# Optimization experiments

Measured on AMD Instinct MI355X. Metric: run time of the kernel, lower is better.

Reference implementation:

```python
import jax, jax.numpy as jnp
import numpy as np

N, D, K = 10000, 784, 16          # nodes, input feat dim, num_neighbors
E = N * (K - 1)                   # edges
H = 128                           # hidden width in all MLPs
SIZES = [784, 128, 2]             # node_sizes


def setup_inputs() -> dict:
    key = jax.random.key(0)
    ks = jax.random.split(key, 24)
    w = lambda k, shape: jax.random.normal(k, shape, jnp.float32) * 0.02
    inp = {
        "x": jax.random.normal(ks[0], (N, D), jnp.float32),
        "edge_attr": jax.random.uniform(ks[1], (E, 1), jnp.float32),
        "idxs": jax.random.randint(ks[2], (N, K - 1), 0, N, dtype=jnp.int32),
    }
    # Layer 1: in=784, msg_size=784, out=128
    inp["l1_msg_w1"] = w(ks[3], (D + 1, H));      inp["l1_msg_b1"] = jnp.zeros((H,), jnp.float32)
    inp["l1_msg_w2"] = w(ks[4], (H, D));          inp["l1_msg_b2"] = jnp.zeros((D,), jnp.float32)
    inp["l1_node_w1"] = w(ks[5], (D + D, H));     inp["l1_node_b1"] = jnp.zeros((H,), jnp.float32)
    inp["l1_node_w2"] = w(ks[6], (H, 128));       inp["l1_node_b2"] = jnp.zeros((128,), jnp.float32)
    # Layer 2: in=128, msg_size=128, out=2
    inp["l2_msg_w1"] = w(ks[7], (128 + 1, H));    inp["l2_msg_b1"] = jnp.zeros((H,), jnp.float32)
    inp["l2_msg_w2"] = w(ks[8], (H, 128));        inp["l2_msg_b2"] = jnp.zeros((128,), jnp.float32)
    inp["l2_node_w1"] = w(ks[9], (128 + 128, H)); inp["l2_node_b1"] = jnp.zeros((H,), jnp.float32)
    inp["l2_node_w2"] = w(ks[10], (H, 2));        inp["l2_node_b2"] = jnp.zeros((2,), jnp.float32)
    return inp


def _mlp(x, w1, b1, w2, b2):
    return jax.nn.relu(x @ w1 + b1) @ w2 + b2


def _node_layer(x, src, edge_attr,
                mw1, mb1, mw2, mb2, nw1, nb1, nw2, nb2):
    # message over edges: cat(x[src], edge_attr) -> MLP   [E, msg_size]
    msg = _mlp(jnp.concatenate([x[src], edge_attr], axis=1), mw1, mb1, mw2, mb2)
    # scatter_mean by src index (faithful to the original, which uses index=src)
    sums = jax.ops.segment_sum(msg, src, num_segments=N)
    cnt = jax.ops.segment_sum(jnp.ones((src.shape[0], 1), msg.dtype), src, num_segments=N)
    agg = jnp.where(cnt > 0, sums / jnp.maximum(cnt, 1.0), 0.0)
    # node update: cat(x, agg_msg) -> MLP
    return _mlp(jnp.concatenate([x, agg], axis=1), nw1, nb1, nw2, nb2)


def reference(x, edge_attr, idxs,
              l1_msg_w1, l1_msg_b1, l1_msg_w2, l1_msg_b2,
              l1_node_w1, l1_node_b1, l1_node_w2, l1_node_b2,
              l2_msg_w1, l2_msg_b1, l2_msg_w2, l2_msg_b2,
              l2_node_w1, l2_node_b1, l2_node_w2, l2_node_b2):
    src = idxs.reshape(-1)  # [E]; dst is unused by the original message computation
    h = _node_layer(x, src, edge_attr,
                    l1_msg_w1, l1_msg_b1, l1_msg_w2, l1_msg_b2,
                    l1_node_w1, l1_node_b1, l1_node_w2, l1_node_b2)
    proj = _node_layer(h, src, edge_attr,
                       l2_msg_w1, l2_msg_b1, l2_msg_w2, l2_msg_b2,
                       l2_node_w1, l2_node_b1, l2_node_w2, l2_node_b2)  # [N, 2]
    # vectorized per-neighbor squared distances (replaces the nested python loop)
    neigh = proj[idxs]                                   # [N, K-1, 2]
    d = jnp.sum((proj[:, None, :] - neigh) ** 2, axis=-1)  # [N, K-1]
    return d.reshape(-1, 1)                              # [N*(K-1), 1]
```

## Files before the change

### kernel.cpp

```cpp
#include <hip/hip_runtime.h>

#define N_NODES 10000
#define E_EDGES 150000
#define KNB     15
#define EBLOCKS 587
#define GEMMB   626

typedef unsigned short u16;
typedef __bf16 bf16x8 __attribute__((ext_vector_type(8)));
typedef float  f32x4  __attribute__((ext_vector_type(4)));

__device__ __forceinline__ void split3(float a, u16& h, u16& m, u16& l) {
    unsigned u = __float_as_uint(a);
    unsigned t = u + 0x7FFFu + ((u >> 16) & 1u);
    h = (u16)(t >> 16);
    float r1 = a - __uint_as_float(t & 0xFFFF0000u);
    unsigned u1 = __float_as_uint(r1);
    m = (u16)(u1 >> 16);
    float r2 = r1 - __uint_as_float(u1 & 0xFFFF0000u);
    l = (u16)(__float_as_uint(r2) >> 16);
}

__global__ void count_kernel(const int* __restrict__ idxs, int* __restrict__ cnt, int e) {
    int i = blockIdx.x * blockDim.x + threadIdx.x;
    if (i < e) atomicAdd(&cnt[idxs[i]], 1);
}

__device__ __forceinline__
void gemm_tile2(const float* __restrict__ A, int K,
                const float* __restrict__ Blo, const float* __restrict__ Bhi, int ldB,
                float* __restrict__ C, int ldC, int M,
                int rowBlk, int colBlk) {
    __shared__ float As2[16][34];
    __shared__ float Bs2[16][64];
    int tid = threadIdx.x;
    int tn  = tid & 15, tm = tid >> 4;
    int arow = tid >> 3, acB = (tid & 7) << 1;
    int brow = tid >> 4, bcol = (tid & 15) << 2;
    int rowBase = rowBlk * 32, colBase = colBlk * 64;

    bool half = (Bhi != nullptr) && (colBase >= 128);
    const float* B = half ? Bhi : Blo;
    int bj = colBase - (half ? 128 : 0) + bcol;

    float2 av; float4 bv;
    auto loadA = [&](int k0, float2& dst) {
        int gr = rowBase + arow;
        if (gr < M) dst = *(const float2*)(A + (size_t)gr * K + k0 + acB);
        else { dst.x = dst.y = 0.f; }
    };
    auto loadB = [&](int k0, float4& dst) {
        dst = *(const float4*)(B + (size_t)(k0 + brow) * ldB + bj);
    };
    loadA(0, av); loadB(0, bv);

    float acc[2][4] = {};
    for (int k0 = 0; k0 < K; k0 += 16) {
        __syncthreads();
        As2[acB + 0][arow] = av.x; As2[acB + 1][arow] = av.y;
        *(float4*)&Bs2[brow][bcol] = bv;
        __syncthreads();
        if (k0 + 16 < K) { loadA(k0 + 16, av); loadB(k0 + 16, bv); }
#pragma unroll
        for (int k = 0; k < 16; ++k) {
            float4 b = *(const float4*)&Bs2[k][tn << 2];
            float2 a = *(const float2*)&As2[k][tm << 1];
            acc[0][0] = fmaf(a.x, b.x, acc[0][0]); acc[0][1] = fmaf(a.x, b.y, acc[0][1]);
            acc[0][2] = fmaf(a.x, b.z, acc[0][2]); acc[0][3] = fmaf(a.x, b.w, acc[0][3]);
            acc[1][0] = fmaf(a.y, b.x, acc[1][0]); acc[1][1] = fmaf(a.y, b.y, acc[1][1]);
            acc[1][2] = fmaf(a.y, b.z, acc[1][2]); acc[1][3] = fmaf(a.y, b.w, acc[1][3]);
        }
    }
#pragma unroll
    for (int i = 0; i < 2; ++i) {
        int row = rowBase + tm * 2 + i;
        if (row >= M) continue;
#pragma unroll
        for (int j = 0; j < 4; ++j)
            C[(size_t)row * ldC + colBase + (tn << 2) + j] = acc[i][j];
    }
}

__global__ __launch_bounds__(256)
void scanfold_kernel(const float* __restrict__ mw2, const float* __restrict__ mb2,
                     const float* __restrict__ nw1, const float* __restrict__ nb2,
                     const float* __restrict__ nw2,
                     const float* __restrict__ m2w1, const float* __restrict__ m2b1,
                     const float* __restrict__ m2w2, const float* __restrict__ m2b2,
                     const float* __restrict__ n2w1, const float* __restrict__ n2b1,
                     float* __restrict__ M1, float* __restrict__ M2,
                     float* __restrict__ WH,
                     float* __restrict__ v1, float* __restrict__ v2,
                     float* __restrict__ bu2, float* __restrict__ bx2,
                     const int* __restrict__ cnt, int* __restrict__ eoff,
                     float* __restrict__ maskv, int* __restrict__ fillc,
                     const float* __restrict__ mw1, u16* __restrict__ Bt) {
    int b = blockIdx.x;
    if (b >= 41) {
        __shared__ float Lt[800][17];
        int b2 = b - 41;
        int colBase = b2 * 16;
        const float* S = (colBase < 128) ? mw1 : nw1;
        int sc = colBase & 127;
        int tid = threadIdx.x;
        for (int i = 0; i < 50; ++i) {
            int row = (tid >> 4) + i * 16;
            Lt[row][tid & 15] = (row < 784) ? S[(size_t)row * 128 + sc + (tid & 15)] : 0.f;
        }
        __syncthreads();
        int col = tid >> 4, o = tid & 15;
        size_t dbase = (size_t)(colBase + col) * 800;
        for (int o2 = o; o2 < 100; o2 += 16) {
            u16 hs[8], ms[8], ls[8];
#pragma unroll
            for (int e = 0; e < 8; ++e) split3(Lt[o2 * 8 + e][col], hs[e], ms[e], ls[e]);
            auto pk = [](const u16* s) {
                uint4 v;
                v.x = s[0] | ((unsigned)s[1] << 16); v.y = s[2] | ((unsigned)s[3] << 16);
                v.z = s[4] | ((unsigned)s[5] << 16); v.w = s[6] | ((unsigned)s[7] << 16);
                return v;
            };
            *(uint4*)(Bt +          dbase + o2 * 8) = pk(hs);
            *(uint4*)(Bt + 204800 + dbase + o2 * 8) = pk(ms);
            *(uint4*)(Bt + 409600 + dbase + o2 * 8) = pk(ls);
        }
        return;
    }
    if (b == 0) {
        __shared__ int ssum[256];
        int tid = threadIdx.x;
        const int CH = 40;
        int base = tid * CH;
        int v[CH]; int s = 0;
#pragma unroll
        for (int q = 0; q < CH; ++q) {
            int i = base + q;
            v[q] = (i < N_NODES) ? cnt[i] : 0;
            s += v[q];
        }
        ssum[tid] = s;
        __syncthreads();
        for (int off = 1; off < 256; off <<= 1) {
            int t = (tid >= off) ? ssum[tid - off] : 0;
            __syncthreads();
            ssum[tid] += t;
            __syncthreads();
        }
        int ex = ssum[tid] - s;
#pragma unroll
        for (int q = 0; q < CH; ++q) {
            int i = base + q;
            if (i < N_NODES) {
                eoff[i]  = ex;
                maskv[i] = (v[q] > 0) ? 1.f : 0.f;
                fillc[i] = 0;
                ex += v[q];
            }
        }
        return;
    }
    b -= 1;
    if (b < 8) {
        gemm_tile2(mw2, 784, nw1 + 784 * 128, nullptr, 128, M1, 128, 128, b >> 1, b & 1);
    } else if (b < 16) {
        int t = b - 8;
        gemm_tile2(m2w2, 128, n2w1 + 128 * 128, nullptr, 128, M2, 128, 128, t >> 1, t & 1);
    } else if (b < 32) {
        int t = b - 16;
        gemm_tile2(nw2, 128, m2w1, n2w1, 128, WH, 256, 128, t >> 2, t & 3);
    } else {
        __shared__ float red[256];
        int t  = (b - 32) >> 1;
        int j  = ((b - 32) & 1) * 64 + (threadIdx.x & 63);
        int kq = threadIdx.x >> 6;
        const float* bvec; const float* Bv; const float* add; float* out; int Kv;
        if (t == 0)      { bvec = mb2;  Bv = nw1 + 784 * 128;  add = nullptr; out = v1;  Kv = 784; }
        else if (t == 1) { bvec = m2b2; Bv = n2w1 + 128 * 128; add = nullptr; out = v2;  Kv = 128; }
        else if (t == 2) { bvec = nb2;  Bv = m2w1;             add = m2b1;    out = bu2; Kv = 128; }
        else             { bvec = nb2;  Bv = n2w1;             add = n2b1;    out = bx2; Kv = 128; }
        float acc = 0.f;
        for (int k = kq; k < Kv; k += 4) acc = fmaf(bvec[k], Bv[k * 128 + j], acc);
        red[threadIdx.x] = acc;
        __syncthreads();
        if (threadIdx.x < 64) {
            float tot = red[threadIdx.x] + red[threadIdx.x + 64] +
                        red[threadIdx.x + 128] + red[threadIdx.x + 192];
            out[j] = tot + (add ? add[j] : 0.f);
        }
    }
}

#define MF(a, b, c) __builtin_amdgcn_mfma_f32_16x16x32_bf16((a), (b), (c), 0, 0, 0)

__device__ __forceinline__
void gemm_mfma(const float* __restrict__ A, const u16* __restrict__ Bt,
               const float* __restrict__ biasLo, const float* __restrict__ biasHi,
               const float* __restrict__ vhi, const float* __restrict__ rowmask,
               float* __restrict__ C, int gb) {
    __shared__ u16 Bs[3][8][64][8];
    __shared__ u16 As[3][2][64][8];
    const int tid  = threadIdx.x;
    const int lane = tid & 63, w = tid >> 6;
    const int rb = gb >> 1, cb = gb & 1;
    const int rowBase = rb * 32, colBase = cb * 128;

    const int ar  = tid >> 3;
    const int akc = (tid & 7) << 2;
    int arow = rowBase + ar; if (arow > N_NODES - 1) arow = N_NODES - 1;
    const float* Ap = A + (size_t)arow * 784;
    const int aL  = (ar & 15) + ((akc >> 3) << 4);
    const int aE  = akc & 4;
    u16* aDst = &As[0][ar >> 4][aL][aE];

    u16* bBase = &Bs[0][0][lane][0];
#define BDEF(j) \
    const int pl##j = (w * 6 + j) >> 3, cf##j = (w * 6 + j) & 7; \
    const int bofs##j = pl##j * 204800 + (colBase + cf##j * 16 + (lane & 15)) * 800 + ((lane >> 4) << 3); \
    const int bd##j = (pl##j * 8 + cf##j) * 512; \
    uint4 bv##j;
    BDEF(0) BDEF(1) BDEF(2) BDEF(3) BDEF(4) BDEF(5)
#undef BDEF

    float4 av;
    ushort4 a3h, a3m, a3l;

#define ALOAD(k0) { int kk = akc + (k0); if (kk >= 784) kk = 0; \
                    av = *(const float4*)(Ap + kk); }
#define BLOADALL(k0) \
    bv0 = *(const uint4*)(Bt + bofs0 + (k0)); \
    bv1 = *(const uint4*)(Bt + bofs1 + (k0)); \
    bv2 = *(const uint4*)(Bt + bofs2 + (k0)); \
    bv3 = *(const uint4*)(Bt + bofs3 + (k0)); \
    bv4 = *(const uint4*)(Bt + bofs4 + (k0)); \
    bv5 = *(const uint4*)(Bt + bofs5 + (k0));
#define ASPLIT() { u16 h, m, l; \
    split3(av.x, h, m, l); a3h.x = h; a3m.x = m; a3l.x = l; \
    split3(av.y, h, m, l); a3h.y = h; a3m.y = m; a3l.y = l; \
    split3(av.z, h, m, l); a3h.z = h; a3m.z = m; a3l.z = l; \
    split3(av.w, h, m, l); a3h.w = h; a3m.w = m; a3l.w = l; }

    f32x4 acc00 = {0.f, 0.f, 0.f, 0.f};
    f32x4 acc01 = acc00, acc10 = acc00, acc11 = acc00;

    ALOAD(0) BLOADALL(0) ASPLIT()

    const u16* aFr = &As[0][0][lane][0];
    const u16* bFr = &Bs[0][w * 2][lane][0];

    for (int t = 0; t < 25; ++t) {
        __syncthreads();
        *(ushort4*)(aDst)        = a3h;
        *(ushort4*)(aDst + 1024) = a3m;
        *(ushort4*)(aDst + 2048) = a3l;
        *(uint4*)(bBase + bd0) = bv0;
        *(uint4*)(bBase + bd1) = bv1;
        *(uint4*)(bBase + bd2) = bv2;
        *(uint4*)(bBase + bd3) = bv3;
        *(uint4*)(bBase + bd4) = bv4;
        *(uint4*)(bBase + bd5) = bv5;
        __syncthreads();
        const int kn = (t + 1) << 5;
        if (t < 24) { ALOAD(kn) BLOADALL(kn) }

        bf16x8 a0h = *(const bf16x8*)(aFr);
        bf16x8 a1h = *(const bf16x8*)(aFr + 512);
        bf16x8 a0m = *(const bf16x8*)(aFr + 1024);
        bf16x8 a1m = *(const bf16x8*)(aFr + 1536);
        bf16x8 a0l = *(const bf16x8*)(aFr + 2048);
        bf16x8 a1l = *(const bf16x8*)(aFr + 2560);

        bf16x8 bb0 = *(const bf16x8*)(bFr);
        bf16x8 bb1 = *(const bf16x8*)(bFr + 512);
        acc00 = MF(a0h, bb0, acc00); acc01 = MF(a0h, bb1, acc01);
        acc10 = MF(a1h, bb0, acc10); acc11 = MF(a1h, bb1, acc11);
        acc00 = MF(a0m, bb0, acc00); acc01 = MF(a0m, bb1, acc01);
        acc10 = MF(a1m, bb0, acc10); acc11 = MF(a1m, bb1, acc11);
        acc00 = MF(a0l, bb0, acc00); acc01 = MF(a0l, bb1, acc01);
        acc10 = MF(a1l, bb0, acc10); acc11 = MF(a1l, bb1, acc11);
        bf16x8 bc0 = *(const bf16x8*)(bFr + 4096);
        bf16x8 bc1 = *(const bf16x8*)(bFr + 4608);
        acc00 = MF(a0h, bc0, acc00); acc01 = MF(a0h, bc1, acc01);
        acc10 = MF(a1h, bc0, acc10); acc11 = MF(a1h, bc1, acc11);
        acc00 = MF(a0m, bc0, acc00); acc01 = MF(a0m, bc1, acc01);
        acc10 = MF(a1m, bc0, acc10); acc11 = MF(a1m, bc1, acc11);
        bf16x8 bdq0 = *(const bf16x8*)(bFr + 8192);
        bf16x8 bdq1 = *(const bf16x8*)(bFr + 8704);
        acc00 = MF(a0h, bdq0, acc00); acc01 = MF(a0h, bdq1, acc01);
        acc10 = MF(a1h, bdq0, acc10); acc11 = MF(a1h, bdq1, acc11);

        if (t < 24) ASPLIT()
    }
#undef ALOAD
#undef BLOADALL
#undef ASPLIT

    const float* bias = cb ? biasHi : biasLo;
#define EPI(rf, cf, ACC) { \
        const int col = colBase + w * 32 + (cf) * 16 + (lane & 15); \
        const int cj  = col & 127; \
        const float bb = bias[cj]; \
        const float vh = cb ? vhi[cj] : 0.f; \
        const int rbase = rowBase + (rf) * 16 + ((lane >> 4) << 2); \
        _Pragma("unroll") \
        for (int r = 0; r < 4; ++r) { \
            int row = rbase + r; \
            if (row < N_NODES) { \
                float v = ACC[r] + bb; \
                if (cb) v = fmaf(rowmask[row], vh, v); \
                C[(size_t)row * 256 + col] = v; \
            } } }
    EPI(0, 0, acc00) EPI(0, 1, acc01) EPI(1, 0, acc10) EPI(1, 1, acc11)
#undef EPI
}

__global__ __launch_bounds__(256)
void fillgemm_kernel(const int* __restrict__ idxs, const float* __restrict__ ea,
                     const int* __restrict__ eoff, int* __restrict__ fillc,
                     float* __restrict__ eas,
                     const float* __restrict__ A, const u16* __restrict__ Bt,
                     const float* __restrict__ biasLo, const float* __restrict__ biasHi,
                     const float* __restrict__ vhi, const float* __restrict__ rowmask,
                     float* __restrict__ C) {
    int gb = blockIdx.x;
    if (gb < GEMMB) {
        gemm_mfma(A, Bt, biasLo, biasHi, vhi, rowmask, C, gb);
        return;
    }
    int i = (gb - GEMMB) * 256 + threadIdx.x;
    if (i < E_EDGES) {
        int s = idxs[i];
        int p = atomicAdd(&fillc[s], 1);
        eas[eoff[s] + p] = ea[i];
    }
}

__global__ __launch_bounds__(512, 4)
void tail16_kernel(const float* __restrict__ UX1, const float* __restrict__ w1last,
                   const float* __restrict__ eas, const int* __restrict__ eoff,
                   const int* __restrict__ cnt, const float* __restrict__ maskv,
                   const float* __restrict__ M1, const float* __restrict__ WH,
                   const float* __restrict__ bu2, const float* __restrict__ bx2,
                   const float* __restrict__ v2,
                   const float* __restrict__ w2last, const float* __restrict__ M2,
                   const float* __restrict__ pw, const float* __restrict__ pb,
                   float* __restrict__ UX2, float* __restrict__ proj) {
    __shared__ float Bs[16][264];
    __shared__ float mhT[128][18];
    __shared__ float ts[16][132];
    __shared__ float ebuf[1024];
    int rowBase = blockIdx.x * 16;
    int tid = threadIdx.x;
    int tr  = tid >> 5;
    int tn  = tid & 31;
    int c4  = tn << 2;

    auto msg_phase = [&](const float* __restrict__ U, const float* __restrict__ wl) {
        int d = tid & 127, grp = tid >> 7;
        float w = wl[d];
        float uu[4], sum[4];
        int es[4], ec[4];
#pragma unroll
        for (int it = 0; it < 4; ++it) {
            int n  = rowBase + it * 4 + grp;
            ec[it] = cnt[n];
            es[it] = eoff[n];
            uu[it] = U[(size_t)n * 256 + d];
            sum[it] = 0.f;
        }
        int ebase = eoff[rowBase];
        int eend  = (rowBase + 16 < N_NODES) ? eoff[rowBase + 16] : E_EDGES;
        for (int w0 = ebase; w0 < eend; w0 += 1024) {
            int wlen = min(1024, eend - w0);
            __syncthreads();
            for (int q = tid; q < wlen; q += 512) ebuf[q] = eas[w0 + q];
            __syncthreads();
#pragma unroll
            for (int it = 0; it < 4; ++it) {
                int lo = max(es[it], w0), hiE = min(es[it] + ec[it], w0 + wlen);
                for (int e = lo; e < hiE; ++e)
                    sum[it] += fmaxf(fmaf(ebuf[e - w0], w, uu[it]), 0.f);
            }
        }
#pragma unroll
        for (int it = 0; it < 4; ++it)
            mhT[d][it * 4 + grp] = (ec[it] > 0) ? sum[it] / (float)ec[it] : 0.f;
    };

    msg_phase(UX1, w1last);

    {
        float a0 = 0.f, a1 = 0.f, a2 = 0.f, a3 = 0.f;
        float4 bv = *(const float4*)(M1 + (size_t)tr * 128 + c4);
        for (int k0 = 0; k0 < 128; k0 += 16) {
            __syncthreads();
            *(float4*)&Bs[tr][c4] = bv;
            __syncthreads();
            if (k0 + 16 < 128)
                bv = *(const float4*)(M1 + (size_t)(k0 + 16 + tr) * 128 + c4);
#pragma unroll
            for (int k = 0; k < 16; ++k) {
                float a = mhT[k0 + k][tr];
                float4 b = *(const float4*)&Bs[k][c4];
                a0 = fmaf(a, b.x, a0); a1 = fmaf(a, b.y, a1);
                a2 = fmaf(a, b.z, a2); a3 = fmaf(a, b.w, a3);
            }
        }
        int row = rowBase + tr;
        float4 xn = *(const float4*)(UX1 + (size_t)row * 256 + 128 + c4);
        float4 o;
        o.x = fmaxf(a0 + xn.x, 0.f);
        o.y = fmaxf(a1 + xn.y, 0.f);
        o.z = fmaxf(a2 + xn.z, 0.f);
        o.w = fmaxf(a3 + xn.w, 0.f);
        *(float4*)&ts[tr][c4] = o;
    }

    {
        float u0 = 0.f, u1 = 0.f, u2 = 0.f, u3 = 0.f;
        float x0 = 0.f, x1 = 0.f, x2 = 0.f, x3 = 0.f;
        int c8 = tn << 3;
        float4 bva = *(const float4*)(WH + (size_t)tr * 256 + c8);
        float4 bvb = *(const float4*)(WH + (size_t)tr * 256 + c8 + 4);
        for (int k0 = 0; k0 < 128; k0 += 16) {
            __syncthreads();
            *(float4*)&Bs[tr][c8]     = bva;
            *(float4*)&Bs[tr][c8 + 4] = bvb;
            __syncthreads();
            if (k0 + 16 < 128) {
                bva = *(const float4*)(WH + (size_t)(k0 + 16 + tr) * 256 + c8);
                bvb = *(const float4*)(WH + (size_t)(k0 + 16 + tr) * 256 + c8 + 4);
            }
#pragma unroll
            for (int k = 0; k < 16; ++k) {
                float a = ts[tr][k0 + k];
                float4 b0 = *(const float4*)&Bs[k][c4];
                float4 b1 = *(const float4*)&Bs[k][c4 + 128];
                u0 = fmaf(a, b0.x, u0); u1 = fmaf(a, b0.y, u1);
                u2 = fmaf(a, b0.z, u2); u3 = fmaf(a, b0.w, u3);
                x0 = fmaf(a, b1.x, x0); x1 = fmaf(a, b1.y, x1);
                x2 = fmaf(a, b1.z, x2); x3 = fmaf(a, b1.w, x3);
            }
        }
        int row = rowBase + tr;
        float rm = maskv[row];
        float4 o0, o1;
        o0.x = u0 + bu2[c4 + 0]; o0.y = u1 + bu2[c4 + 1];
        o0.z = u2 + bu2[c4 + 2]; o0.w = u3 + bu2[c4 + 3];
        o1.x = fmaf(rm, v2[c4 + 0], x0 + bx2[c4 + 0]);
        o1.y = fmaf(rm, v2[c4 + 1], x1 + bx2[c4 + 1]);
        o1.z = fmaf(rm, v2[c4 + 2], x2 + bx2[c4 + 2]);
        o1.w = fmaf(rm, v2[c4 + 3], x3 + bx2[c4 + 3]);
        float* orow = UX2 + (size_t)row * 256;
        *(float4*)(orow + c4)       = o0;
        *(float4*)(orow + 128 + c4) = o1;
    }
    __syncthreads();

    msg_phase(UX2, w2last);

    {
        float a0 = 0.f, a1 = 0.f, a2 = 0.f, a3 = 0.f;
        float4 bv = *(const float4*)(M2 + (size_t)tr * 128 + c4);
        for (int k0 = 0; k0 < 128; k0 += 16) {
            __syncthreads();
            *(float4*)&Bs[tr][c4] = bv;
            __syncthreads();
            if (k0 + 16 < 128)
                bv = *(const float4*)(M2 + (size_t)(k0 + 16 + tr) * 128 + c4);
#pragma unroll
            for (int k = 0; k < 16; ++k) {
                float a = mhT[k0 + k][tr];
                float4 b = *(const float4*)&Bs[k][c4];
                a0 = fmaf(a, b.x, a0); a1 = fmaf(a, b.y, a1);
                a2 = fmaf(a, b.z, a2); a3 = fmaf(a, b.w, a3);
            }
        }
        int row = rowBase + tr;
        float4 xn = *(const float4*)(UX2 + (size_t)row * 256 + 128 + c4);
        float t0 = fmaxf(a0 + xn.x, 0.f);
        float t1 = fmaxf(a1 + xn.y, 0.f);
        float t2 = fmaxf(a2 + xn.z, 0.f);
        float t3 = fmaxf(a3 + xn.w, 0.f);
        float pp0 = fmaf(t3, pw[2*(c4+3)],   fmaf(t2, pw[2*(c4+2)],   fmaf(t1, pw[2*(c4+1)],   t0 * pw[2*c4])));
        float pp1 = fmaf(t3, pw[2*(c4+3)+1], fmaf(t2, pw[2*(c4+2)+1], fmaf(t1, pw[2*(c4+1)+1], t0 * pw[2*c4+1])));
        for (int off = 16; off > 0; off >>= 1) {
            pp0 += __shfl_xor(pp0, off, 64);
            pp1 += __shfl_xor(pp1, off, 64);
        }
        if (tn == 0) {
            proj[2 * row]     = pp0 + pb[0];
            proj[2 * row + 1] = pp1 + pb[1];
        }
    }
}

__global__ void dist_kernel(const float* __restrict__ proj, const int* __restrict__ idxs,
                            float* __restrict__ out, int e) {
    int i = blockIdx.x * blockDim.x + threadIdx.x;
    if (i >= e) return;
    int n = i / KNB;
    int m = idxs[i];
    float2 pn = *(const float2*)(proj + 2 * n);
    float2 pm = *(const float2*)(proj + 2 * m);
    float dx = pn.x - pm.x;
    float dy = pn.y - pm.y;
    out[i] = dx * dx + dy * dy;
}

extern "C" void kernel_launch(void* const* d_in, const int* in_sizes, int n_in,
                              void* d_out, int out_size, void* d_ws, size_t ws_size,
                              hipStream_t stream) {
    (void)in_sizes; (void)n_in; (void)out_size; (void)ws_size;
    const float* x    = (const float*)d_in[0];
    const float* eatt = (const float*)d_in[1];
    const int*   idxs = (const int*)d_in[2];
    const float* mw1  = (const float*)d_in[3];
    const float* mb1  = (const float*)d_in[4];
    const float* mw2  = (const float*)d_in[5];
    const float* mb2  = (const float*)d_in[6];
    const float* nw1  = (const float*)d_in[7];
    const float* nb1  = (const float*)d_in[8];
    const float* nw2  = (const float*)d_in[9];
    const float* nb2  = (const float*)d_in[10];
    const float* m2w1 = (const float*)d_in[11];
    const float* m2b1 = (const float*)d_in[12];
    const float* m2w2 = (const float*)d_in[13];
    const float* m2b2 = (const float*)d_in[14];
    const float* n2w1 = (const float*)d_in[15];
    const float* n2b1 = (const float*)d_in[16];
    const float* n2w2 = (const float*)d_in[17];
    const float* n2b2 = (const float*)d_in[18];
    float* out = (float*)d_out;

    float* fws   = (float*)d_ws;
    float* UX1   = fws;
    float* UX2   = fws + 2560000;
    float* proj  = fws + 5120000;
    float* maskv = fws + 5140000;
    float* eas   = fws + 5150016;
    float* M1    = fws + 5300016;
    float* M2    = fws + 5316400;
    float* WH    = fws + 5332784;
    float* v1    = fws + 5365552;
    float* v2    = fws + 5365680;
    float* bu2   = fws + 5365808;
    float* bx2   = fws + 5365936;
    int*   cnt   = (int*)(fws + 5366064);
    int*   fillc = cnt + N_NODES;
    int*   eoff  = fillc + N_NODES;
    u16*   Bt    = (u16*)(fws + 2560000);

    hipMemsetAsync(cnt, 0, N_NODES * sizeof(int), stream);
    count_kernel<<<EBLOCKS, 256, 0, stream>>>(idxs, cnt, E_EDGES);

    scanfold_kernel<<<57, 256, 0, stream>>>(mw2, mb2, nw1, nb2, nw2,
                                            m2w1, m2b1, m2w2, m2b2, n2w1, n2b1,
                                            M1, M2, WH, v1, v2, bu2, bx2,
                                            cnt, eoff, maskv, fillc, mw1, Bt);

    fillgemm_kernel<<<GEMMB + EBLOCKS, 256, 0, stream>>>(
        idxs, eatt, eoff, fillc, eas,
        x, Bt, mb1, nb1, v1, maskv, UX1);

    tail16_kernel<<<625, 512, 0, stream>>>(UX1, mw1 + 784 * 128, eas, eoff, cnt, maskv,
                                           M1, WH, bu2, bx2, v2,
                                           m2w1 + 128 * 128, M2,
                                           n2w2, n2b2,
                                           UX2, proj);

    dist_kernel<<<EBLOCKS, 256, 0, stream>>>(proj, idxs, out, E_EDGES);
}
```

Measured before the change: 252.0 us.

## Halve GEMM column tile and load B directly to LDS via global_load_lds

The split-bf16 MFMA GEMM tile goes from 32x128 to 32x64 columns, which doubles the block count so more blocks share the work. Each wave now computes one 16-column fragment for two row fragments. B fragments are copied straight from global to LDS with global_load_lds, with no register staging. Launch bounds request 4 blocks per CU. The smaller tile lowers LDS use and register pressure, but each A tile is loaded and split twice as often, and the direct LDS copy is no longer prefetched one iteration ahead, so its load latency sits between the two barriers.

```diff
diff --git a/kernel.cpp b/kernel.cpp
--- a/kernel.cpp
+++ b/kernel.cpp
@@ -4,7 +4,9 @@
 #define E_EDGES 150000
 #define KNB     15
 #define EBLOCKS 587
-#define GEMMB   626
+#define GEMMB   1252
+#define KPAD    800
+#define PLSTR   204800
 
 typedef unsigned short u16;
 typedef __bf16 bf16x8 __attribute__((ext_vector_type(8)));
@@ -19,6 +21,13 @@
     m = (u16)(u1 >> 16);
     float r2 = r1 - __uint_as_float(u1 & 0xFFFF0000u);
     l = (u16)(__float_as_uint(r2) >> 16);
+}
+
+__device__ __forceinline__ void gl_lds16(const u16* g, u16* l) {
+    __builtin_amdgcn_global_load_lds(
+        (const __attribute__((address_space(1))) unsigned int*)(g),
+        (__attribute__((address_space(3))) unsigned int*)(l),
+        16, 0, 0);
 }
 
 __global__ void count_kernel(const int* __restrict__ idxs, int* __restrict__ cnt, int e) {
@@ -97,7 +106,7 @@
                      const float* __restrict__ mw1, u16* __restrict__ Bt) {
     int b = blockIdx.x;
     if (b >= 41) {
-        __shared__ float Lt[800][17];
+        __shared__ float Lt[KPAD][17];
         int b2 = b - 41;
         int colBase = b2 * 16;
         const float* S = (colBase < 128) ? mw1 : nw1;
@@ -109,7 +118,7 @@
         }
         __syncthreads();
         int col = tid >> 4, o = tid & 15;
-        size_t dbase = (size_t)(colBase + col) * 800;
+        size_t dbase = (size_t)(colBase + col) * KPAD;
         for (int o2 = o; o2 < 100; o2 += 16) {
             u16 hs[8], ms[8], ls[8];
 #pragma unroll
@@ -120,9 +129,9 @@
                 v.z = s[4] | ((unsigned)s[5] << 16); v.w = s[6] | ((unsigned)s[7] << 16);
                 return v;
             };
-            *(uint4*)(Bt +          dbase + o2 * 8) = pk(hs);
-            *(uint4*)(Bt + 204800 + dbase + o2 * 8) = pk(ms);
-            *(uint4*)(Bt + 409600 + dbase + o2 * 8) = pk(ls);
+            *(uint4*)(Bt +           dbase + o2 * 8) = pk(hs);
+            *(uint4*)(Bt + PLSTR   + dbase + o2 * 8) = pk(ms);
+            *(uint4*)(Bt + 2*PLSTR + dbase + o2 * 8) = pk(ls);
         }
         return;
     }
@@ -197,123 +206,110 @@
                const float* __restrict__ biasLo, const float* __restrict__ biasHi,
                const float* __restrict__ vhi, const float* __restrict__ rowmask,
                float* __restrict__ C, int gb) {
-    __shared__ u16 Bs[3][8][64][8];
     __shared__ u16 As[3][2][64][8];
+    __shared__ u16 Bs[3][4][64][8];
     const int tid  = threadIdx.x;
     const int lane = tid & 63, w = tid >> 6;
-    const int rb = gb >> 1, cb = gb & 1;
-    const int rowBase = rb * 32, colBase = cb * 128;
-
-    const int ar  = tid >> 3;
-    const int akc = (tid & 7) << 2;
-    int arow = rowBase + ar; if (arow > N_NODES - 1) arow = N_NODES - 1;
+    const int rb = gb >> 2, cbq = gb & 3;
+    const int rowBase = rb * 32, colBase = cbq * 64;
+    const bool hi = cbq >= 2;
+    u16* const AsB = &As[0][0][0][0];
+    u16* const BsB = &Bs[0][0][0][0];
+
+    const int srf   = w & 1;
+    const int chunk = ((w >> 1) << 2) + (lane >> 4);
+    const int aoff  = chunk << 2;
+    int arow = rowBase + srf * 16 + (lane & 15);
+    if (arow > N_NODES - 1) arow = N_NODES - 1;
     const float* Ap = A + (size_t)arow * 784;
-    const int aL  = (ar & 15) + ((akc >> 3) << 4);
-    const int aE  = akc & 4;
-    u16* aDst = &As[0][ar >> 4][aL][aE];
-
-    u16* bBase = &Bs[0][0][lane][0];
-#define BDEF(j) \
-    const int pl##j = (w * 6 + j) >> 3, cf##j = (w * 6 + j) & 7; \
-    const int bofs##j = pl##j * 204800 + (colBase + cf##j * 16 + (lane & 15)) * 800 + ((lane >> 4) << 3); \
-    const int bd##j = (pl##j * 8 + cf##j) * 512; \
-    uint4 bv##j;
-    BDEF(0) BDEF(1) BDEF(2) BDEF(3) BDEF(4) BDEF(5)
-#undef BDEF
+    u16* aDst = AsB + srf * 512 + (((lane & 15) + ((chunk >> 1) << 4)) << 3)
+                    + ((chunk & 1) << 2);
+
+#define BSRC(c) ((size_t)((c) >> 2) * PLSTR + \
+                 (size_t)(colBase + (((c) & 3) << 4) + (lane & 15)) * KPAD + \
+                 ((lane >> 4) << 3))
+    const int c0 = w * 3, c1 = w * 3 + 1, c2 = w * 3 + 2;
+    const u16* bsrc0 = Bt + BSRC(c0);
+    const u16* bsrc1 = Bt + BSRC(c1);
+    const u16* bsrc2 = Bt + BSRC(c2);
+    u16* bd0 = BsB + c0 * 512;
+    u16* bd1 = BsB + c1 * 512;
+    u16* bd2 = BsB + c2 * 512;
+#undef BSRC
 
     float4 av;
     ushort4 a3h, a3m, a3l;
 
-#define ALOAD(k0) { int kk = akc + (k0); if (kk >= 784) kk = 0; \
-                    av = *(const float4*)(Ap + kk); }
-#define BLOADALL(k0) \
-    bv0 = *(const uint4*)(Bt + bofs0 + (k0)); \
-    bv1 = *(const uint4*)(Bt + bofs1 + (k0)); \
-    bv2 = *(const uint4*)(Bt + bofs2 + (k0)); \
-    bv3 = *(const uint4*)(Bt + bofs3 + (k0)); \
-    bv4 = *(const uint4*)(Bt + bofs4 + (k0)); \
-    bv5 = *(const uint4*)(Bt + bofs5 + (k0));
+#define ALOAD(k0) { int kk = (k0) + aoff; \
+    if (kk < 784) av = *(const float4*)(Ap + kk); \
+    else { av.x = av.y = av.z = av.w = 0.f; } }
 #define ASPLIT() { u16 h, m, l; \
     split3(av.x, h, m, l); a3h.x = h; a3m.x = m; a3l.x = l; \
     split3(av.y, h, m, l); a3h.y = h; a3m.y = m; a3l.y = l; \
     split3(av.z, h, m, l); a3h.z = h; a3m.z = m; a3l.z = l; \
     split3(av.w, h, m, l); a3h.w = h; a3m.w = m; a3l.w = l; }
 
-    f32x4 acc00 = {0.f, 0.f, 0.f, 0.f};
-    f32x4 acc01 = acc00, acc10 = acc00, acc11 = acc00;
-
-    ALOAD(0) BLOADALL(0) ASPLIT()
-
-    const u16* aFr = &As[0][0][lane][0];
-    const u16* bFr = &Bs[0][w * 2][lane][0];
+    f32x4 acc0 = {0.f, 0.f, 0.f, 0.f};
+    f32x4 acc1 = acc0;
+
+    const u16* aFr = AsB + (lane << 3);
+    const u16* bFr = BsB + (w << 9) + (lane << 3);
+
+    ALOAD(0) ASPLIT()
 
     for (int t = 0; t < 25; ++t) {
         __syncthreads();
+        const int k0 = t << 5;
+        gl_lds16(bsrc0 + k0, bd0);
+        gl_lds16(bsrc1 + k0, bd1);
+        gl_lds16(bsrc2 + k0, bd2);
         *(ushort4*)(aDst)        = a3h;
         *(ushort4*)(aDst + 1024) = a3m;
         *(ushort4*)(aDst + 2048) = a3l;
-        *(uint4*)(bBase + bd0) = bv0;
-        *(uint4*)(bBase + bd1) = bv1;
-        *(uint4*)(bBase + bd2) = bv2;
-        *(uint4*)(bBase + bd3) = bv3;
-        *(uint4*)(bBase + bd4) = bv4;
-        *(uint4*)(bBase + bd5) = bv5;
-        __syncthreads();
-        const int kn = (t + 1) << 5;
-        if (t < 24) { ALOAD(kn) BLOADALL(kn) }
-
-        bf16x8 a0h = *(const bf16x8*)(aFr);
-        bf16x8 a1h = *(const bf16x8*)(aFr + 512);
-        bf16x8 a0m = *(const bf16x8*)(aFr + 1024);
-        bf16x8 a1m = *(const bf16x8*)(aFr + 1536);
-        bf16x8 a0l = *(const bf16x8*)(aFr + 2048);
-        bf16x8 a1l = *(const bf16x8*)(aFr + 2560);
-
-        bf16x8 bb0 = *(const bf16x8*)(bFr);
-        bf16x8 bb1 = *(const bf16x8*)(bFr + 512);
-        acc00 = MF(a0h, bb0, acc00); acc01 = MF(a0h, bb1, acc01);
-        acc10 = MF(a1h, bb0, acc10); acc11 = MF(a1h, bb1, acc11);
-        acc00 = MF(a0m, bb0, acc00); acc01 = MF(a0m, bb1, acc01);
-        acc10 = MF(a1m, bb0, acc10); acc11 = MF(a1m, bb1, acc11);
-        acc00 = MF(a0l, bb0, acc00); acc01 = MF(a0l, bb1, acc01);
-        acc10 = MF(a1l, bb0, acc10); acc11 = MF(a1l, bb1, acc11);
-        bf16x8 bc0 = *(const bf16x8*)(bFr + 4096);
-        bf16x8 bc1 = *(const bf16x8*)(bFr + 4608);
-        acc00 = MF(a0h, bc0, acc00); acc01 = MF(a0h, bc1, acc01);
-        acc10 = MF(a1h, bc0, acc10); acc11 = MF(a1h, bc1, acc11);
-        acc00 = MF(a0m, bc0, acc00); acc01 = MF(a0m, bc1, acc01);
-        acc10 = MF(a1m, bc0, acc10); acc11 = MF(a1m, bc1, acc11);
-        bf16x8 bdq0 = *(const bf16x8*)(bFr + 8192);
-        bf16x8 bdq1 = *(const bf16x8*)(bFr + 8704);
-        acc00 = MF(a0h, bdq0, acc00); acc01 = MF(a0h, bdq1, acc01);
-        acc10 = MF(a1h, bdq0, acc10); acc11 = MF(a1h, bdq1, acc11);
-
+        __syncthreads();
+        if (t < 24) ALOAD((t + 1) << 5)
+        {
+            bf16x8 a0h = *(const bf16x8*)(aFr);
+            bf16x8 a1h = *(const bf16x8*)(aFr + 512);
+            bf16x8 a0m = *(const bf16x8*)(aFr + 1024);
+            bf16x8 a1m = *(const bf16x8*)(aFr + 1536);
+            bf16x8 a0l = *(const bf16x8*)(aFr + 2048);
+            bf16x8 a1l = *(const bf16x8*)(aFr + 2560);
+            bf16x8 bh  = *(const bf16x8*)(bFr);
+            bf16x8 bm  = *(const bf16x8*)(bFr + 2048);
+            bf16x8 bl  = *(const bf16x8*)(bFr + 4096);
+            acc0 = MF(a0h, bh, acc0); acc1 = MF(a1h, bh, acc1);
+            acc0 = MF(a0m, bh, acc0); acc1 = MF(a1m, bh, acc1);
+            acc0 = MF(a0l, bh, acc0); acc1 = MF(a1l, bh, acc1);
+            acc0 = MF(a0h, bm, acc0); acc1 = MF(a1h, bm, acc1);
+            acc0 = MF(a0m, bm, acc0); acc1 = MF(a1m, bm, acc1);
+            acc0 = MF(a0h, bl, acc0); acc1 = MF(a1h, bl, acc1);
+        }
         if (t < 24) ASPLIT()
     }
 #undef ALOAD
-#undef BLOADALL
 #undef ASPLIT
 
-    const float* bias = cb ? biasHi : biasLo;
-#define EPI(rf, cf, ACC) { \
-        const int col = colBase + w * 32 + (cf) * 16 + (lane & 15); \
+    const float* bias = hi ? biasHi : biasLo;
+#define EPI(rf, ACC) { \
+        const int col = colBase + w * 16 + (lane & 15); \
         const int cj  = col & 127; \
         const float bb = bias[cj]; \
-        const float vh = cb ? vhi[cj] : 0.f; \
+        const float vh = hi ? vhi[cj] : 0.f; \
         const int rbase = rowBase + (rf) * 16 + ((lane >> 4) << 2); \
         _Pragma("unroll") \
-        for (int r = 0; r < 4; ++r) { \
-            int row = rbase + r; \
+        for (int rr = 0; rr < 4; ++rr) { \
+            int row = rbase + rr; \
             if (row < N_NODES) { \
-                float v = ACC[r] + bb; \
-                if (cb) v = fmaf(rowmask[row], vh, v); \
+                float v = ACC[rr] + bb; \
+                if (hi) v = fmaf(rowmask[row], vh, v); \
                 C[(size_t)row * 256 + col] = v; \
             } } }
-    EPI(0, 0, acc00) EPI(0, 1, acc01) EPI(1, 0, acc10) EPI(1, 1, acc11)
+    EPI(0, acc0) EPI(1, acc1)
 #undef EPI
 }
 
-__global__ __launch_bounds__(256)
+__global__ __launch_bounds__(256, 4)
 void fillgemm_kernel(const int* __restrict__ idxs, const float* __restrict__ ea,
                      const int* __restrict__ eoff, int* __restrict__ fillc,
                      float* __restrict__ eas,
```

Result: faster. 245.4 us (median of 2 runs) (-2.6%).
